# Performance work log

Measured on AMD Instinct MI355X. Metric: run time of the kernel, lower is better.

The kernel has to match this reference:

```python
import jax, jax.numpy as jnp
import numpy as np

N_MC = 32
DT = 0.1
HIDDEN = 64
PROSPECTIVE_STEPS = 3
# scan_steps=3 -> first 3 of the hard-coded velocities
VELOCITIES = np.array([[0.2, 0.0], [0.0, 0.2], [0.15, 0.15]], dtype=np.float32)


def linear_interp_1d(x, out_size):
    """F.interpolate(mode='linear', align_corners=False) on last axis. x: [..., N]."""
    n = x.shape[-1]
    scale = n / out_size
    pos = (jnp.arange(out_size, dtype=x.dtype) + 0.5) * scale - 0.5
    pos = jnp.clip(pos, 0.0, n - 1)
    lo = jnp.floor(pos).astype(jnp.int32)
    hi = jnp.minimum(lo + 1, n - 1)
    w = pos - lo.astype(x.dtype)
    return x[..., lo] * (1.0 - w) + x[..., hi] * w


def setup_inputs() -> dict:
    key = jax.random.key(0)
    ks = jax.random.split(key, 8)
    B = 16384
    image = jax.random.uniform(ks[0], (B, 28, 28), dtype=jnp.float32)
    s = 1.0 / np.sqrt(N_MC)
    W_ff = jax.random.normal(ks[1], (N_MC, N_MC), dtype=jnp.float32) * s
    W_fb = jax.random.normal(ks[2], (N_MC, N_MC), dtype=jnp.float32) * s
    W_vel = jax.random.normal(ks[3], (N_MC, 2), dtype=jnp.float32) * s
    Wc1 = jax.random.normal(ks[4], (HIDDEN, 4 * N_MC), dtype=jnp.float32) * (1.0 / np.sqrt(4 * N_MC))
    bc1 = jnp.zeros((HIDDEN,), dtype=jnp.float32)
    Wc2 = jax.random.normal(ks[5], (10, HIDDEN), dtype=jnp.float32) * (1.0 / np.sqrt(HIDDEN))
    bc2 = jnp.zeros((10,), dtype=jnp.float32)
    return {"image": image, "W_ff": W_ff, "W_fb": W_fb, "W_vel": W_vel,
            "Wc1": Wc1, "bc1": bc1, "Wc2": Wc2, "bc2": bc2}


def _column_features(image, W_ff, W_fb, W_vel):
    B = image.shape[0]
    flat = image.reshape(B, -1)                       # [B, 784]
    flat_t = jnp.swapaxes(image, 1, 2).reshape(B, -1)  # transpose(0,1) per image
    sensory = linear_interp_1d(flat, N_MC) * 80.0     # [B, n_mc]
    topdown = linear_interp_1d(flat_t, N_MC) * 40.0   # [B, n_mc]

    r6 = jnp.zeros_like(sensory)                      # reset_state per image
    y_fb = jax.nn.relu(topdown @ W_fb.T)              # top-down feedback drive
    for v in VELOCITIES:                              # fixed 3-step scan
        vel_in = W_vel @ jnp.asarray(v)               # [n_mc]
        for _ in range(PROSPECTIVE_STEPS):            # fixed 3 prospective steps
            pred = r6 @ W_fb.T                        # top-down prediction of sensory drive
            eps_pos = jax.nn.relu(sensory - pred)
            eps_neg = jax.nn.relu(pred - sensory)
            y_ff = jax.nn.relu((eps_pos - eps_neg) @ W_ff.T)
            r6 = r6 + DT * (-r6 + y_ff + y_fb + vel_in)  # leaky L6 integrator
    feature = jnp.concatenate([y_ff, y_fb, r6, eps_pos + eps_neg], axis=-1)  # [B, 4*n_mc]
    return feature


def reference(image, W_ff, W_fb, W_vel, Wc1, bc1, Wc2, bc2):
    feature = jax.lax.stop_gradient(_column_features(image, W_ff, W_fb, W_vel))
    h = jax.nn.gelu(feature @ Wc1.T + bc1, approximate=False)
    logits = h @ Wc2.T + bc2                          # [B, 10]
    return logits
```

## Files before the change

kernel.cpp:

```cpp
#include <hip/hip_runtime.h>
#include <math.h>

typedef _Float16 f16x8 __attribute__((ext_vector_type(8)));
typedef float    f32x4 __attribute__((ext_vector_type(4)));

#define SCRW 132

__device__ __forceinline__ f32x4 mfma16(f16x8 a, f16x8 b, f32x4 c) {
  return __builtin_amdgcn_mfma_f32_16x16x32_f16(a, b, c, 0, 0, 0);
}

__device__ __forceinline__ void splitA(f32x4 a0, f32x4 a1, f16x8& hi, f16x8& lo) {
#pragma unroll
  for (int j = 0; j < 4; ++j) {
    float x0 = a0[j], x1 = a1[j];
    _Float16 h0 = (_Float16)x0, h1 = (_Float16)x1;
    hi[j] = h0; hi[j + 4] = h1;
    lo[j]     = (_Float16)(x0 - (float)h0);
    lo[j + 4] = (_Float16)(x1 - (float)h1);
  }
}

__device__ __forceinline__ f16x8 bfrag8(const float* p) {
  const f32x4* q = (const f32x4*)p;
  f32x4 w0 = q[0], w1 = q[1];
  f16x8 b;
#pragma unroll
  for (int j = 0; j < 4; ++j) { b[j] = (_Float16)w0[j]; b[j + 4] = (_Float16)w1[j]; }
  return b;
}

__global__ __launch_bounds__(256) void mnist_cols(
    const float* __restrict__ img,  const float* __restrict__ Wff,
    const float* __restrict__ Wfb,  const float* __restrict__ Wvel,
    const float* __restrict__ Wc1,  const float* __restrict__ bc1,
    const float* __restrict__ Wc2,  const float* __restrict__ bc2,
    float* __restrict__ out) {
  __shared__ float scr_all[4][16 * SCRW];
  const int tid = threadIdx.x;
  const int wv = tid >> 6, l = tid & 63;
  const int g = l >> 4, c0 = l & 15, c1 = c0 + 16;
  float* scr = scr_all[wv];
  const int s0 = blockIdx.x * 64 + wv * 16;

  const float pos0 = 24.5f * (float)c0 + 11.75f;
  const float pos1 = 24.5f * (float)c1 + 11.75f;
  const int lo0 = (int)pos0, lo1 = (int)pos1;
  const float w0 = pos0 - (float)lo0, w1 = pos1 - (float)lo1;
  const int ta0 = (lo0 % 28) * 28 + lo0 / 28;
  const int tb0 = ((lo0 + 1) % 28) * 28 + (lo0 + 1) / 28;
  const int ta1 = (lo1 % 28) * 28 + lo1 / 28;
  const int tb1 = ((lo1 + 1) % 28) * 28 + (lo1 + 1) / 28;

  float sens[4][2], td[4][2];
#pragma unroll
  for (int r = 0; r < 4; ++r) {
    const float* base = img + (size_t)(s0 + g * 4 + r) * 784;
    float sa0 = base[lo0], sa1 = base[lo0 + 1];
    float sb0 = base[lo1], sb1 = base[lo1 + 1];
    float t00 = base[ta0], t01 = base[tb0];
    float t10 = base[ta1], t11 = base[tb1];
    sens[r][0] = (sa0 * (1.0f - w0) + sa1 * w0) * 80.0f;
    sens[r][1] = (sb0 * (1.0f - w1) + sb1 * w1) * 80.0f;
    td[r][0]   = (t00 * (1.0f - w0) + t01 * w0) * 40.0f;
    td[r][1]   = (t10 * (1.0f - w1) + t11 * w1) * 40.0f;
  }

  f16x8 bfb0 = bfrag8(Wfb + c0 * 32 + g * 8);
  f16x8 bfb1 = bfrag8(Wfb + c1 * 32 + g * 8);
  f16x8 bff0 = bfrag8(Wff + c0 * 32 + g * 8);
  f16x8 bff1 = bfrag8(Wff + c1 * 32 + g * 8);

  const float wva0 = Wvel[c0 * 2], wva1 = Wvel[c0 * 2 + 1];
  const float wvb0 = Wvel[c1 * 2], wvb1 = Wvel[c1 * 2 + 1];

  const f32x4 zero = {0.f, 0.f, 0.f, 0.f};
  f16x8 ahi, alo;

#pragma unroll
  for (int r = 0; r < 4; ++r) {
    int row = (g * 4 + r) * SCRW;
    scr[row + c0] = td[r][0];
    scr[row + c1] = td[r][1];
  }
  {
    const f32x4* ap = (const f32x4*)(scr + c0 * SCRW + g * 8);
    splitA(ap[0], ap[1], ahi, alo);
  }
  f32x4 afb0 = mfma16(alo, bfb0, mfma16(ahi, bfb0, zero));
  f32x4 afb1 = mfma16(alo, bfb1, mfma16(ahi, bfb1, zero));
  float yfb[4][2];
#pragma unroll
  for (int r = 0; r < 4; ++r) {
    yfb[r][0] = fmaxf(afb0[r], 0.f);
    yfb[r][1] = fmaxf(afb1[r], 0.f);
  }

  float r6[4][2] = {};
  float d[4][2], yff[4][2];
  const float VX[3] = {0.2f, 0.0f, 0.15f};
  const float VY[3] = {0.0f, 0.2f, 0.15f};
#pragma unroll
  for (int v = 0; v < 3; ++v) {
    float vin[2];
    vin[0] = wva0 * VX[v] + wva1 * VY[v];
    vin[1] = wvb0 * VX[v] + wvb1 * VY[v];
#pragma unroll
    for (int st = 0; st < 3; ++st) {
#pragma unroll
      for (int r = 0; r < 4; ++r) {
        int row = (g * 4 + r) * SCRW;
        scr[row + c0] = r6[r][0];
        scr[row + c1] = r6[r][1];
      }
      {
        const f32x4* ap = (const f32x4*)(scr + c0 * SCRW + g * 8);
        splitA(ap[0], ap[1], ahi, alo);
      }
      f32x4 p0 = mfma16(alo, bfb0, mfma16(ahi, bfb0, zero));
      f32x4 p1 = mfma16(alo, bfb1, mfma16(ahi, bfb1, zero));
#pragma unroll
      for (int r = 0; r < 4; ++r) {
        d[r][0] = sens[r][0] - p0[r];
        d[r][1] = sens[r][1] - p1[r];
      }
#pragma unroll
      for (int r = 0; r < 4; ++r) {
        int row = (g * 4 + r) * SCRW;
        scr[row + c0] = d[r][0];
        scr[row + c1] = d[r][1];
      }
      {
        const f32x4* ap = (const f32x4*)(scr + c0 * SCRW + g * 8);
        splitA(ap[0], ap[1], ahi, alo);
      }
      f32x4 q0 = mfma16(alo, bff0, mfma16(ahi, bff0, zero));
      f32x4 q1 = mfma16(alo, bff1, mfma16(ahi, bff1, zero));
#pragma unroll
      for (int r = 0; r < 4; ++r) {
        yff[r][0] = fmaxf(q0[r], 0.f);
        yff[r][1] = fmaxf(q1[r], 0.f);
#pragma unroll
        for (int cb = 0; cb < 2; ++cb)
          r6[r][cb] = r6[r][cb] + 0.1f * (yff[r][cb] - r6[r][cb] + yfb[r][cb] + vin[cb]);
      }
    }
  }

#pragma unroll
  for (int r = 0; r < 4; ++r) {
    int row = (g * 4 + r) * SCRW;
    scr[row +      c0] = yff[r][0];        scr[row +      c1] = yff[r][1];
    scr[row + 32 + c0] = yfb[r][0];        scr[row + 32 + c1] = yfb[r][1];
    scr[row + 64 + c0] = r6[r][0];         scr[row + 64 + c1] = r6[r][1];
    scr[row + 96 + c0] = fabsf(d[r][0]);   scr[row + 96 + c1] = fabsf(d[r][1]);
  }
  f32x4 acc0 = zero, acc1 = zero, acc2 = zero, acc3 = zero;
#pragma unroll
  for (int kb = 0; kb < 4; ++kb) {
    const f32x4* ap = (const f32x4*)(scr + c0 * SCRW + kb * 32 + g * 8);
    f16x8 fhi, flo;
    splitA(ap[0], ap[1], fhi, flo);
    const int ko = kb * 32 + g * 8;
    f16x8 b0 = bfrag8(Wc1 + (size_t)(0 * 16 + c0) * 128 + ko);
    f16x8 b1 = bfrag8(Wc1 + (size_t)(1 * 16 + c0) * 128 + ko);
    f16x8 b2 = bfrag8(Wc1 + (size_t)(2 * 16 + c0) * 128 + ko);
    f16x8 b3 = bfrag8(Wc1 + (size_t)(3 * 16 + c0) * 128 + ko);
    acc0 = mfma16(flo, b0, mfma16(fhi, b0, acc0));
    acc1 = mfma16(flo, b1, mfma16(fhi, b1, acc1));
    acc2 = mfma16(flo, b2, mfma16(fhi, b2, acc2));
    acc3 = mfma16(flo, b3, mfma16(fhi, b3, acc3));
  }
  float h[4][4];
  const float B0 = bc1[c0], B1 = bc1[16 + c0], B2 = bc1[32 + c0], B3 = bc1[48 + c0];
#pragma unroll
  for (int r = 0; r < 4; ++r) {
    float x0 = acc0[r] + B0, x1 = acc1[r] + B1, x2 = acc2[r] + B2, x3 = acc3[r] + B3;
    h[r][0] = 0.5f * x0 * (1.0f + erff(x0 * 0.70710678118654752f));
    h[r][1] = 0.5f * x1 * (1.0f + erff(x1 * 0.70710678118654752f));
    h[r][2] = 0.5f * x2 * (1.0f + erff(x2 * 0.70710678118654752f));
    h[r][3] = 0.5f * x3 * (1.0f + erff(x3 * 0.70710678118654752f));
  }

#pragma unroll
  for (int r = 0; r < 4; ++r) {
    int row = (g * 4 + r) * SCRW;
#pragma unroll
    for (int nb = 0; nb < 4; ++nb) scr[row + nb * 16 + c0] = h[r][nb];
  }
  f32x4 accL = zero;
#pragma unroll
  for (int kb = 0; kb < 2; ++kb) {
    const f32x4* ap = (const f32x4*)(scr + c0 * SCRW + kb * 32 + g * 8);
    f16x8 hhi, hlo;
    splitA(ap[0], ap[1], hhi, hlo);
    f16x8 b;
    if (c0 < 10) {
      b = bfrag8(Wc2 + (size_t)c0 * 64 + kb * 32 + g * 8);
    } else {
#pragma unroll
      for (int j = 0; j < 8; ++j) b[j] = (_Float16)0.f;
    }
    accL = mfma16(hlo, b, mfma16(hhi, b, accL));
  }
  if (c0 < 10) {
    const float bb = bc2[c0];
#pragma unroll
    for (int r = 0; r < 4; ++r)
      out[(size_t)(s0 + g * 4 + r) * 10 + c0] = accL[r] + bb;
  }
}

extern "C" void kernel_launch(void* const* d_in, const int* in_sizes, int n_in,
                              void* d_out, int out_size, void* d_ws, size_t ws_size,
                              hipStream_t stream) {
  const float* img  = (const float*)d_in[0];
  const float* Wff  = (const float*)d_in[1];
  const float* Wfb  = (const float*)d_in[2];
  const float* Wvel = (const float*)d_in[3];
  const float* Wc1  = (const float*)d_in[4];
  const float* bc1  = (const float*)d_in[5];
  const float* Wc2  = (const float*)d_in[6];
  const float* bc2  = (const float*)d_in[7];
  float* out = (float*)d_out;
  const int B = in_sizes[0] / 784;
  const int grid = B / 64;
  hipLaunchKernelGGL(mnist_cols, dim3(grid), dim3(256), 0, stream,
                     img, Wff, Wfb, Wvel, Wc1, bc1, Wc2, bc2, out);
}
```

Measured before the change: 24.26 us.

## Fold W_ff·W_fb into one recurrence matmul and stage image rows through LDS

Rewrites the recurrence algebraically: since y_ff = relu(W_ff(sens - W_fb r6)), it precomputes M = W_ff·W_fb and W_ff·sens, so each step needs one split-precision matmul instead of two. The final eps is recomputed only on the last step. Image rows are streamed into LDS per wave in 16-byte chunks via global_load_lds instead of scattered global gathers. It also adds a third split-fp16 correction term on the weights, which costs extra MFMAs. The precomputed product may change rounding behaviour.

```diff
diff --git a/kernel.cpp b/kernel.cpp
--- a/kernel.cpp
+++ b/kernel.cpp
@@ -5,19 +5,35 @@
 typedef float    f32x4 __attribute__((ext_vector_type(4)));
 
 #define SCRW 132
+#define IMG_F 784
+#define CHUNK_F 3136
+
+typedef __attribute__((address_space(3))) void lds_void;
+typedef const __attribute__((address_space(1))) void glb_void;
 
 __device__ __forceinline__ f32x4 mfma16(f16x8 a, f16x8 b, f32x4 c) {
   return __builtin_amdgcn_mfma_f32_16x16x32_f16(a, b, c, 0, 0, 0);
 }
 
-__device__ __forceinline__ void splitA(f32x4 a0, f32x4 a1, f16x8& hi, f16x8& lo) {
+__device__ __forceinline__ void splitP(const float* p, f16x8& hi, f16x8& lo) {
+  const f32x4* q = (const f32x4*)p;
+  f32x4 a0 = q[0], a1 = q[1];
 #pragma unroll
   for (int j = 0; j < 4; ++j) {
-    float x0 = a0[j], x1 = a1[j];
-    _Float16 h0 = (_Float16)x0, h1 = (_Float16)x1;
+    _Float16 h0 = (_Float16)a0[j], h1 = (_Float16)a1[j];
     hi[j] = h0; hi[j + 4] = h1;
-    lo[j]     = (_Float16)(x0 - (float)h0);
-    lo[j + 4] = (_Float16)(x1 - (float)h1);
+    lo[j]     = (_Float16)(a0[j] - (float)h0);
+    lo[j + 4] = (_Float16)(a1[j] - (float)h1);
+  }
+}
+
+__device__ __forceinline__ void splitS(const float* p, int stride, f16x8& hi, f16x8& lo) {
+#pragma unroll
+  for (int j = 0; j < 8; ++j) {
+    float x = p[j * stride];
+    _Float16 h = (_Float16)x;
+    hi[j] = h;
+    lo[j] = (_Float16)(x - (float)h);
   }
 }
 
@@ -28,6 +44,15 @@
 #pragma unroll
   for (int j = 0; j < 4; ++j) { b[j] = (_Float16)w0[j]; b[j + 4] = (_Float16)w1[j]; }
   return b;
+}
+
+__device__ __forceinline__ void load_chunk(const float* gsrc, float* lbase, int l) {
+#pragma unroll
+  for (int i = 0; i < 12; ++i)
+    __builtin_amdgcn_global_load_lds((glb_void*)(gsrc + i * 256 + l * 4),
+                                     (lds_void*)(lbase + i * 256), 16, 0, 0);
+  __builtin_amdgcn_global_load_lds((glb_void*)(gsrc + 3072 + l),
+                                   (lds_void*)(lbase + 3072), 4, 0, 0);
 }
 
 __global__ __launch_bounds__(256) void mnist_cols(
@@ -36,11 +61,14 @@
     const float* __restrict__ Wc1,  const float* __restrict__ bc1,
     const float* __restrict__ Wc2,  const float* __restrict__ bc2,
     float* __restrict__ out) {
+  __shared__ float img_lds[4][CHUNK_F];
   __shared__ float scr_all[4][16 * SCRW];
+
   const int tid = threadIdx.x;
   const int wv = tid >> 6, l = tid & 63;
   const int g = l >> 4, c0 = l & 15, c1 = c0 + 16;
-  float* scr = scr_all[wv];
+  float* scr  = scr_all[wv];
+  float* ibuf = img_lds[wv];
   const int s0 = blockIdx.x * 64 + wv * 16;
 
   const float pos0 = 24.5f * (float)c0 + 11.75f;
@@ -52,52 +80,82 @@
   const int ta1 = (lo1 % 28) * 28 + lo1 / 28;
   const int tb1 = ((lo1 + 1) % 28) * 28 + (lo1 + 1) / 28;
 
-  float sens[4][2], td[4][2];
-#pragma unroll
-  for (int r = 0; r < 4; ++r) {
-    const float* base = img + (size_t)(s0 + g * 4 + r) * 784;
-    float sa0 = base[lo0], sa1 = base[lo0 + 1];
-    float sb0 = base[lo1], sb1 = base[lo1 + 1];
-    float t00 = base[ta0], t01 = base[tb0];
-    float t10 = base[ta1], t11 = base[tb1];
-    sens[r][0] = (sa0 * (1.0f - w0) + sa1 * w0) * 80.0f;
-    sens[r][1] = (sb0 * (1.0f - w1) + sb1 * w1) * 80.0f;
-    td[r][0]   = (t00 * (1.0f - w0) + t01 * w0) * 40.0f;
-    td[r][1]   = (t10 * (1.0f - w1) + t11 * w1) * 40.0f;
-  }
-
-  f16x8 bfb0 = bfrag8(Wfb + c0 * 32 + g * 8);
-  f16x8 bfb1 = bfrag8(Wfb + c1 * 32 + g * 8);
-  f16x8 bff0 = bfrag8(Wff + c0 * 32 + g * 8);
-  f16x8 bff1 = bfrag8(Wff + c1 * 32 + g * 8);
-
+  f16x8 bfbh0, bfbl0, bfbh1, bfbl1, bffh0, bffl0, bffh1, bffl1;
+  splitP(Wfb + c0 * 32 + g * 8, bfbh0, bfbl0);
+  splitP(Wfb + c1 * 32 + g * 8, bfbh1, bfbl1);
+  splitP(Wff + c0 * 32 + g * 8, bffh0, bffl0);
+  splitP(Wff + c1 * 32 + g * 8, bffh1, bffl1);
+  f16x8 afbh0, afbl0, afbh1, afbl1;
+  splitS(Wfb + g * 256 + c0,      32, afbh0, afbl0);
+  splitS(Wfb + g * 256 + c0 + 16, 32, afbh1, afbl1);
   const float wva0 = Wvel[c0 * 2], wva1 = Wvel[c0 * 2 + 1];
   const float wvb0 = Wvel[c1 * 2], wvb1 = Wvel[c1 * 2 + 1];
 
+  load_chunk(img + (size_t)s0 * IMG_F, ibuf, l);
+
   const f32x4 zero = {0.f, 0.f, 0.f, 0.f};
+  f32x4 m00 = mfma16(afbh0, bffl0, mfma16(afbl0, bffh0, mfma16(afbh0, bffh0, zero)));
+  f32x4 m01 = mfma16(afbh0, bffl1, mfma16(afbl0, bffh1, mfma16(afbh0, bffh1, zero)));
+  f32x4 m10 = mfma16(afbh1, bffl0, mfma16(afbl1, bffh0, mfma16(afbh1, bffh0, zero)));
+  f32x4 m11 = mfma16(afbh1, bffl1, mfma16(afbl1, bffh1, mfma16(afbh1, bffh1, zero)));
+#pragma unroll
+  for (int r = 0; r < 4; ++r) {
+    scr[(g * 4 + r) * 32 + c0]            = m00[r];
+    scr[(g * 4 + r) * 32 + c0 + 16]       = m01[r];
+    scr[(16 + g * 4 + r) * 32 + c0]       = m10[r];
+    scr[(16 + g * 4 + r) * 32 + c0 + 16]  = m11[r];
+  }
+  f16x8 mbh0, mbl0, mbh1, mbl1;
+  splitS(scr + g * 256 + c0,      32, mbh0, mbl0);
+  splitS(scr + g * 256 + c0 + 16, 32, mbh1, mbl1);
+
+  float sens[4][2] = {}, td[4][2] = {};
+#pragma unroll
+  for (int c = 0; c < 4; ++c) {
+    asm volatile("s_waitcnt vmcnt(0)" ::: "memory");
+    __builtin_amdgcn_sched_barrier(0);
+    if (g == c) {
+#pragma unroll
+      for (int r = 0; r < 4; ++r) {
+        const float* base = ibuf + r * IMG_F;
+        float sa0 = base[lo0], sa1 = base[lo0 + 1];
+        float sb0 = base[lo1], sb1 = base[lo1 + 1];
+        float t00 = base[ta0], t01 = base[tb0];
+        float t10 = base[ta1], t11 = base[tb1];
+        sens[r][0] = (sa0 * (1.0f - w0) + sa1 * w0) * 80.0f;
+        sens[r][1] = (sb0 * (1.0f - w1) + sb1 * w1) * 80.0f;
+        td[r][0]   = (t00 * (1.0f - w0) + t01 * w0) * 40.0f;
+        td[r][1]   = (t10 * (1.0f - w1) + t11 * w1) * 40.0f;
+      }
+    }
+    if (c < 3) load_chunk(img + (size_t)(s0 + (c + 1) * 4) * IMG_F, ibuf, l);
+  }
+
   f16x8 ahi, alo;
-
 #pragma unroll
   for (int r = 0; r < 4; ++r) {
     int row = (g * 4 + r) * SCRW;
     scr[row + c0] = td[r][0];
     scr[row + c1] = td[r][1];
   }
-  {
-    const f32x4* ap = (const f32x4*)(scr + c0 * SCRW + g * 8);
-    splitA(ap[0], ap[1], ahi, alo);
-  }
-  f32x4 afb0 = mfma16(alo, bfb0, mfma16(ahi, bfb0, zero));
-  f32x4 afb1 = mfma16(alo, bfb1, mfma16(ahi, bfb1, zero));
+  splitP(scr + c0 * SCRW + g * 8, ahi, alo);
+  f32x4 f0 = mfma16(ahi, bfbl0, mfma16(alo, bfbh0, mfma16(ahi, bfbh0, zero)));
+  f32x4 f1 = mfma16(ahi, bfbl1, mfma16(alo, bfbh1, mfma16(ahi, bfbh1, zero)));
   float yfb[4][2];
 #pragma unroll
-  for (int r = 0; r < 4; ++r) {
-    yfb[r][0] = fmaxf(afb0[r], 0.f);
-    yfb[r][1] = fmaxf(afb1[r], 0.f);
-  }
-
-  float r6[4][2] = {};
-  float d[4][2], yff[4][2];
+  for (int r = 0; r < 4; ++r) { yfb[r][0] = fmaxf(f0[r], 0.f); yfb[r][1] = fmaxf(f1[r], 0.f); }
+
+#pragma unroll
+  for (int r = 0; r < 4; ++r) {
+    int row = (g * 4 + r) * SCRW;
+    scr[row + c0] = sens[r][0];
+    scr[row + c1] = sens[r][1];
+  }
+  splitP(scr + c0 * SCRW + g * 8, ahi, alo);
+  f32x4 sff0 = mfma16(ahi, bffl0, mfma16(alo, bffh0, mfma16(ahi, bffh0, zero)));
+  f32x4 sff1 = mfma16(ahi, bffl1, mfma16(alo, bffh1, mfma16(ahi, bffh1, zero)));
+
+  float r6[4][2] = {}, d[4][2] = {}, yff[4][2] = {};
   const float VX[3] = {0.2f, 0.0f, 0.15f};
   const float VY[3] = {0.0f, 0.2f, 0.15f};
 #pragma unroll
@@ -110,39 +168,24 @@
 #pragma unroll
       for (int r = 0; r < 4; ++r) {
         int row = (g * 4 + r) * SCRW;
-        scr[row + c0] = r6[r][0];
-        scr[row + c1] = r6[r][1];
-      }
-      {
-        const f32x4* ap = (const f32x4*)(scr + c0 * SCRW + g * 8);
-        splitA(ap[0], ap[1], ahi, alo);
-      }
-      f32x4 p0 = mfma16(alo, bfb0, mfma16(ahi, bfb0, zero));
-      f32x4 p1 = mfma16(alo, bfb1, mfma16(ahi, bfb1, zero));
+        scr[row + c0] = -r6[r][0];
+        scr[row + c1] = -r6[r][1];
+      }
+      splitP(scr + c0 * SCRW + g * 8, ahi, alo);
+      f32x4 y0 = mfma16(ahi, mbl0, mfma16(alo, mbh0, mfma16(ahi, mbh0, sff0)));
+      f32x4 y1 = mfma16(ahi, mbl1, mfma16(alo, mbh1, mfma16(ahi, mbh1, sff1)));
+      if (v == 2 && st == 2) {
+        f32x4 t0 = mfma16(ahi, bfbl0, mfma16(alo, bfbh0, mfma16(ahi, bfbh0, zero)));
+        f32x4 t1 = mfma16(ahi, bfbl1, mfma16(alo, bfbh1, mfma16(ahi, bfbh1, zero)));
+#pragma unroll
+        for (int r = 0; r < 4; ++r) { d[r][0] = sens[r][0] + t0[r]; d[r][1] = sens[r][1] + t1[r]; }
+      }
 #pragma unroll
       for (int r = 0; r < 4; ++r) {
-        d[r][0] = sens[r][0] - p0[r];
-        d[r][1] = sens[r][1] - p1[r];
-      }
-#pragma unroll
-      for (int r = 0; r < 4; ++r) {
-        int row = (g * 4 + r) * SCRW;
-        scr[row + c0] = d[r][0];
-        scr[row + c1] = d[r][1];
-      }
-      {
-        const f32x4* ap = (const f32x4*)(scr + c0 * SCRW + g * 8);
-        splitA(ap[0], ap[1], ahi, alo);
-      }
-      f32x4 q0 = mfma16(alo, bff0, mfma16(ahi, bff0, zero));
-      f32x4 q1 = mfma16(alo, bff1, mfma16(ahi, bff1, zero));
-#pragma unroll
-      for (int r = 0; r < 4; ++r) {
-        yff[r][0] = fmaxf(q0[r], 0.f);
-        yff[r][1] = fmaxf(q1[r], 0.f);
-#pragma unroll
-        for (int cb = 0; cb < 2; ++cb)
-          r6[r][cb] = r6[r][cb] + 0.1f * (yff[r][cb] - r6[r][cb] + yfb[r][cb] + vin[cb]);
+        yff[r][0] = fmaxf(y0[r], 0.f);
+        yff[r][1] = fmaxf(y1[r], 0.f);
+        r6[r][0] += 0.1f * (yff[r][0] - r6[r][0] + yfb[r][0] + vin[0]);
+        r6[r][1] += 0.1f * (yff[r][1] - r6[r][1] + yfb[r][1] + vin[1]);
       }
     }
   }
@@ -158,14 +201,13 @@
   f32x4 acc0 = zero, acc1 = zero, acc2 = zero, acc3 = zero;
 #pragma unroll
   for (int kb = 0; kb < 4; ++kb) {
-    const f32x4* ap = (const f32x4*)(scr + c0 * SCRW + kb * 32 + g * 8);
     f16x8 fhi, flo;
-    splitA(ap[0], ap[1], fhi, flo);
+    splitP(scr + c0 * SCRW + kb * 32 + g * 8, fhi, flo);
     const int ko = kb * 32 + g * 8;
-    f16x8 b0 = bfrag8(Wc1 + (size_t)(0 * 16 + c0) * 128 + ko);
-    f16x8 b1 = bfrag8(Wc1 + (size_t)(1 * 16 + c0) * 128 + ko);
-    f16x8 b2 = bfrag8(Wc1 + (size_t)(2 * 16 + c0) * 128 + ko);
-    f16x8 b3 = bfrag8(Wc1 + (size_t)(3 * 16 + c0) * 128 + ko);
+    f16x8 b0 = bfrag8(Wc1 + (size_t)(c0)      * 128 + ko);
+    f16x8 b1 = bfrag8(Wc1 + (size_t)(16 + c0) * 128 + ko);
+    f16x8 b2 = bfrag8(Wc1 + (size_t)(32 + c0) * 128 + ko);
+    f16x8 b3 = bfrag8(Wc1 + (size_t)(48 + c0) * 128 + ko);
     acc0 = mfma16(flo, b0, mfma16(fhi, b0, acc0));
     acc1 = mfma16(flo, b1, mfma16(fhi, b1, acc1));
     acc2 = mfma16(flo, b2, mfma16(fhi, b2, acc2));
@@ -191,9 +233,8 @@
   f32x4 accL = zero;
 #pragma unroll
   for (int kb = 0; kb < 2; ++kb) {
-    const f32x4* ap = (const f32x4*)(scr + c0 * SCRW + kb * 32 + g * 8);
     f16x8 hhi, hlo;
-    splitA(ap[0], ap[1], hhi, hlo);
+    splitP(scr + c0 * SCRW + kb * 32 + g * 8, hhi, hlo);
     f16x8 b;
     if (c0 < 10) {
       b = bfrag8(Wc2 + (size_t)c0 * 64 + kb * 32 + g * 8);
```

Measured after the change: 24.36 us. No clear change (+0.4%).
